# Performance work log

Measured on AMD Instinct MI355X. Metric: run time of the kernel, lower is better.

The kernel has to match this reference:

```python
import jax, jax.numpy as jnp
import numpy as np

N_HEADS = 16
ROPE_BASE = 10000.0


def _rotate_half(x):
    x1, x2 = jnp.split(x, 2, axis=-1)
    return jnp.concatenate([-x2, x1], axis=-1)


def _rope_cos_sin(positions, d_k, dtype):
    # standard YaRN-style rotary tables (attention scale mscale = 1.0)
    inv_freq = 1.0 / (ROPE_BASE ** (jnp.arange(0, d_k, 2, dtype=jnp.float32) / d_k))
    freqs = positions.astype(jnp.float32)[:, None] * inv_freq[None, :]  # [T, d_k/2]
    emb = jnp.concatenate([freqs, freqs], axis=-1)                      # [T, d_k]
    return jnp.cos(emb).astype(dtype), jnp.sin(emb).astype(dtype)


def setup_inputs() -> dict:
    key = jax.random.key(0)
    ks = jax.random.split(key, 8)
    B, T, D = 1, 2048, 1024
    s = 0.02
    return {
        "query": jax.random.normal(ks[0], (B, T, D), jnp.float32),
        "key": jax.random.normal(ks[1], (B, T, D), jnp.float32),
        "value": jax.random.normal(ks[2], (B, T, D), jnp.float32),
        "yarn_positions": jnp.arange(T, dtype=jnp.int32),
        "wq": jax.random.normal(ks[3], (D, D), jnp.float32) * s,
        "wk": jax.random.normal(ks[4], (D, D), jnp.float32) * s,
        "wv": jax.random.normal(ks[5], (D, D), jnp.float32) * s,
        "wo_w": jax.random.normal(ks[6], (D, D), jnp.float32) * s,
        "wo_b": jnp.zeros((D,), jnp.float32),
    }


def reference(query, key, value, yarn_positions, wq, wk, wv, wo_w, wo_b):
    B, Tq, D = query.shape
    Tk = key.shape[1]
    H = N_HEADS
    dk = D // H

    # nn.Linear(bias=False): y = x @ W.T
    Q = (query @ wq.T).reshape(B, Tq, H, dk).transpose(0, 2, 1, 3)  # [B,H,Tq,dk]
    K = (key @ wk.T).reshape(B, Tk, H, dk).transpose(0, 2, 1, 3)
    V = (value @ wv.T).reshape(B, Tk, H, dk).transpose(0, 2, 1, 3)

    # YaRN rotary position embedding on Q and K (same positions for q and k)
    cos, sin = _rope_cos_sin(yarn_positions, dk, Q.dtype)  # [T, dk]
    cos = cos[None, None, :, :]
    sin = sin[None, None, :, :]
    Q = Q * cos + _rotate_half(Q) * sin
    K = K * cos + _rotate_half(K) * sin

    scale = 1.0 / jnp.sqrt(jnp.asarray(dk, Q.dtype))
    scores = jnp.einsum('bhqd,bhkd->bhqk', Q, K) * scale  # [B,H,Tq,Tk]

    # causal mask (is_causal=True)
    causal = jnp.triu(jnp.ones((Tq, Tk), dtype=bool), 1)
    scores = jnp.where(causal[None, None], -jnp.inf, scores)

    attn = jax.nn.softmax(scores, axis=-1)
    out = jnp.einsum('bhqk,bhkd->bhqd', attn, V)
    out = out.transpose(0, 2, 1, 3).reshape(B, Tq, D)
    return out @ wo_w.T + wo_b
```

## Files before the change

kernel.cpp:

```cpp
#include <hip/hip_runtime.h>
#include <hip/hip_bf16.h>
#include <stdint.h>

#define TT 2048
#define DD 1024
#define NH 16
#define DK 64

typedef __attribute__((ext_vector_type(8))) short bf16x8;
typedef __attribute__((ext_vector_type(4))) float f32x4;
typedef __attribute__((ext_vector_type(8))) unsigned short u16x8;
typedef __attribute__((ext_vector_type(4))) unsigned short u16x4;

__device__ __forceinline__ unsigned short f2bf(float f) {
  union { float f; unsigned u; } x; x.f = f;
  unsigned r = (x.u + 0x7FFFu + ((x.u >> 16) & 1u)) >> 16;
  return (unsigned short)r;
}

__device__ __forceinline__ void gload16(const void* g, void* l) {
  __builtin_amdgcn_global_load_lds(
      (const __attribute__((address_space(1))) unsigned int*)g,
      (__attribute__((address_space(3))) unsigned int*)l, 16, 0, 0);
}

__global__ __launch_bounds__(256) void cvt_all(
    const float* __restrict__ q, const float* __restrict__ k, const float* __restrict__ v,
    const float* __restrict__ wq, const float* __restrict__ wk, const float* __restrict__ wv,
    const float* __restrict__ wo,
    unsigned short* __restrict__ oq, unsigned short* __restrict__ ok, unsigned short* __restrict__ ov,
    unsigned short* __restrict__ owq, unsigned short* __restrict__ owk, unsigned short* __restrict__ owv,
    unsigned short* __restrict__ owo) {
  int b = blockIdx.x;
  const float* src; unsigned short* dst; int sb;
  if (b < 1024)      { src = q;  dst = oq;  sb = b; }
  else if (b < 2048) { src = k;  dst = ok;  sb = b - 1024; }
  else if (b < 3072) { src = v;  dst = ov;  sb = b - 2048; }
  else if (b < 3584) { src = wq; dst = owq; sb = b - 3072; }
  else if (b < 4096) { src = wk; dst = owk; sb = b - 3584; }
  else if (b < 4608) { src = wv; dst = owv; sb = b - 4096; }
  else               { src = wo; dst = owo; sb = b - 4608; }
  size_t i0 = (size_t)sb * 2048 + (size_t)threadIdx.x * 8;
  f32x4 a = *(const f32x4*)(src + i0);
  f32x4 c = *(const f32x4*)(src + i0 + 4);
  u16x8 r;
#pragma unroll
  for (int j = 0; j < 4; ++j) { r[j] = f2bf(a[j]); r[j + 4] = f2bf(c[j]); }
  *(u16x8*)(dst + i0) = r;
}

__global__ __launch_bounds__(256) void rope_tab(const int* __restrict__ pos,
                                                float* __restrict__ cosT,
                                                float* __restrict__ sinT) {
  int idx = blockIdx.x * 256 + threadIdx.x;
  int t = idx >> 5, i = idx & 31;
  float inv = exp2f((float)i * -0.41524101186092028f);
  float ang = (float)pos[t] * inv;
  cosT[idx] = cosf(ang);
  sinT[idx] = sinf(ang);
}

__global__ __launch_bounds__(256) void gemm_qkv(
    const unsigned short* __restrict__ xq, const unsigned short* __restrict__ xk,
    const unsigned short* __restrict__ xv,
    const unsigned short* __restrict__ wqb, const unsigned short* __restrict__ wkb,
    const unsigned short* __restrict__ wvb,
    unsigned short* __restrict__ QF, unsigned short* __restrict__ KF,
    unsigned short* __restrict__ VF,
    const float* __restrict__ cosT, const float* __restrict__ sinT) {
  __shared__ unsigned short Ash[128 * 64];
  __shared__ unsigned short Bsh[128 * 64];
  const int z = blockIdx.z;
  const unsigned short* A = (z == 0) ? xq : (z == 1) ? xk : xv;
  const unsigned short* W = (z == 0) ? wqb : (z == 1) ? wkb : wvb;
  const int brow = blockIdx.x * 128;
  const int bcol = blockIdx.y * 128;
  const int tid = threadIdx.x;
  const int lane = tid & 63;
  const int w = tid >> 6;
  const int wr = w >> 1, wc = w & 1;
  const char* Ab = (const char*)A + (size_t)brow * (DD * 2);
  const char* Wb = (const char*)W + (size_t)bcol * (DD * 2);
  char* AshB = (char*)Ash;
  char* BshB = (char*)Bsh;
  f32x4 acc[4][4];
#pragma unroll
  for (int mi = 0; mi < 4; ++mi)
#pragma unroll
    for (int ni = 0; ni < 4; ++ni)
#pragma unroll
      for (int r = 0; r < 4; ++r) acc[mi][ni][r] = 0.0f;

  for (int k0 = 0; k0 < DD; k0 += 64) {
    __syncthreads();
#pragma unroll
    for (int it = 0; it < 4; ++it) {
      int c = it * 256 + tid;
      int row = c >> 3;
      int xb = (c & 7) << 4;
      int sxb = xb ^ ((row & 7) << 4);
      int ldso = (it * 256 + (tid & 192)) << 4;
      gload16(Ab + (size_t)row * (DD * 2) + k0 * 2 + sxb, AshB + ldso);
      gload16(Wb + (size_t)row * (DD * 2) + k0 * 2 + sxb, BshB + ldso);
    }
    __syncthreads();
#pragma unroll
    for (int ks = 0; ks < 2; ++ks) {
      bf16x8 af[4], bfr[4];
      int colb = ks * 64 + ((lane >> 4) << 4);
#pragma unroll
      for (int mi = 0; mi < 4; ++mi) {
        int row = wr * 64 + mi * 16 + (lane & 15);
        af[mi] = *(const bf16x8*)(AshB + row * 128 + (colb ^ ((row & 7) << 4)));
      }
#pragma unroll
      for (int ni = 0; ni < 4; ++ni) {
        int row = wc * 64 + ni * 16 + (lane & 15);
        bfr[ni] = *(const bf16x8*)(BshB + row * 128 + (colb ^ ((row & 7) << 4)));
      }
#pragma unroll
      for (int mi = 0; mi < 4; ++mi)
#pragma unroll
        for (int ni = 0; ni < 4; ++ni)
          acc[mi][ni] = __builtin_amdgcn_mfma_f32_16x16x32_bf16(af[mi], bfr[ni], acc[mi][ni], 0, 0, 0);
    }
  }

  const int hcol = bcol + wc * 64;
  const int h = hcol >> 6;
  if (z == 0) {
    const float sc = 0.18033688011112042f;
#pragma unroll
    for (int mi = 0; mi < 4; ++mi) {
#pragma unroll
      for (int r = 0; r < 4; ++r) {
        int t = brow + wr * 64 + mi * 16 + ((lane >> 4) << 2) + r;
        int qw_ = t >> 5, mif = (t >> 4) & 1, r16 = t & 15;
        size_t fb = (((size_t)(h * 64 + qw_) * 2 + mif) * 2) * 1024;
#pragma unroll
        for (int ni = 0; ni < 2; ++ni) {
          int dl = ni * 16 + (lane & 15);
          float cv = cosT[t * 32 + dl];
          float sv = sinT[t * 32 + dl];
          float x1 = acc[mi][ni][r];
          float x2 = acc[mi][ni + 2][r];
          size_t off = fb + (size_t)(r16 + 16 * (dl >> 3)) * 16 + (dl & 7) * 2;
          *(unsigned short*)((char*)QF + off) = f2bf((x1 * cv - x2 * sv) * sc);
          *(unsigned short*)((char*)QF + off + 1024) = f2bf((x2 * cv + x1 * sv) * sc);
        }
      }
    }
  } else if (z == 1) {
#pragma unroll
    for (int mi = 0; mi < 4; ++mi) {
#pragma unroll
      for (int r = 0; r < 4; ++r) {
        int t = brow + wr * 64 + mi * 16 + ((lane >> 4) << 2) + r;
        int kt = t >> 6, nif = (t >> 4) & 3, r16 = t & 15;
        size_t fb = (((size_t)(h * 32 + kt) * 2) * 4 + nif) * 1024;
#pragma unroll
        for (int ni = 0; ni < 2; ++ni) {
          int dl = ni * 16 + (lane & 15);
          float cv = cosT[t * 32 + dl];
          float sv = sinT[t * 32 + dl];
          float x1 = acc[mi][ni][r];
          float x2 = acc[mi][ni + 2][r];
          size_t off = fb + (size_t)(r16 + 16 * (dl >> 3)) * 16 + (dl & 7) * 2;
          *(unsigned short*)((char*)KF + off) = f2bf(x1 * cv - x2 * sv);
          *(unsigned short*)((char*)KF + off + 4096) = f2bf(x2 * cv + x1 * sv);
        }
      }
    }
  } else {
#pragma unroll
    for (int mi = 0; mi < 4; ++mi) {
      int t0 = brow + wr * 64 + mi * 16 + ((lane >> 4) << 2);
      int kt = t0 >> 6, ksf = (t0 & 63) >> 5, slot = (t0 & 31) >> 3, j0 = t0 & 7;
#pragma unroll
      for (int ni = 0; ni < 4; ++ni) {
        int dh = ni * 16 + (lane & 15);
        int lanef = (dh & 15) + 16 * slot;
        int nif = dh >> 4;
        size_t off = ((((size_t)(h * 32 + kt) * 2 + ksf) * 4 + nif) * 64 + lanef) * 16 + j0 * 2;
        u16x4 pk;
#pragma unroll
        for (int r = 0; r < 4; ++r) pk[r] = f2bf(acc[mi][ni][r]);
        *(u16x4*)((char*)VF + off) = pk;
      }
    }
  }
}

__global__ __launch_bounds__(256, 2) void attn_fa(
    const unsigned short* __restrict__ QF, const unsigned short* __restrict__ KF,
    const unsigned short* __restrict__ VF, unsigned short* __restrict__ AO) {
  __shared__ char LB[26624];
  __shared__ float MR[4][32];
  const int tid = threadIdx.x;
  const int lane = tid & 63;
  const int w = tid >> 6;
  const int bid = blockIdx.x;
  const int xcd = bid & 7;
  const int idx = bid >> 3;
  const int h = xcd * 2 + (idx & 1);
  const int qw = 63 - (idx >> 1);
  const int q0w = qw * 32;
  const int NT = (qw >> 1) + 1;
  char* PshB = LB + w * 4096;
  const char* Kb = (const char*)KF + (size_t)h * 32 * 8192;
  const char* Vb = (const char*)VF + (size_t)h * 32 * 8192;

  bf16x8 qf[2][2];
  {
    const char* Qb = (const char*)QF + (size_t)(h * 64 + qw) * 4096;
#pragma unroll
    for (int mi = 0; mi < 2; ++mi)
#pragma unroll
      for (int ks = 0; ks < 2; ++ks)
        qf[mi][ks] = *(const bf16x8*)(Qb + (mi * 2 + ks) * 1024 + lane * 16);
  }

  bf16x8 vone;
#pragma unroll
  for (int j = 0; j < 8; ++j) vone[j] = (short)0x3F80;

  f32x4 accO[2][5];
  float mrow[2];
#pragma unroll
  for (int mi = 0; mi < 2; ++mi) {
    mrow[mi] = -1e30f;
#pragma unroll
    for (int ni = 0; ni < 5; ++ni)
#pragma unroll
      for (int r = 0; r < 4; ++r) accO[mi][ni][r] = 0.0f;
  }

  bf16x8 kfA[2][4], kfB[2][4], vf[2][4];
  {
    int kt0 = (w < NT) ? w : 0;
    const char* p = Kb + (size_t)kt0 * 8192 + lane * 16;
#pragma unroll
    for (int ks = 0; ks < 2; ++ks)
#pragma unroll
      for (int ni = 0; ni < 4; ++ni)
        kfA[ks][ni] = *(const bf16x8*)(p + (ks * 4 + ni) * 1024);
  }

  for (int kt = w; kt < NT; kt += 4) {
    {
      const char* p = Vb + (size_t)kt * 8192 + lane * 16;
#pragma unroll
      for (int ks = 0; ks < 2; ++ks)
#pragma unroll
        for (int ni = 0; ni < 4; ++ni)
          vf[ks][ni] = *(const bf16x8*)(p + (ks * 4 + ni) * 1024);
    }
    f32x4 s[2][4];
#pragma unroll
    for (int mi = 0; mi < 2; ++mi)
#pragma unroll
      for (int ni = 0; ni < 4; ++ni)
#pragma unroll
        for (int r = 0; r < 4; ++r) s[mi][ni][r] = 0.0f;
    __builtin_amdgcn_s_setprio(1);
#pragma unroll
    for (int ks = 0; ks < 2; ++ks)
#pragma unroll
      for (int mi = 0; mi < 2; ++mi)
#pragma unroll
        for (int ni = 0; ni < 4; ++ni)
          s[mi][ni] = __builtin_amdgcn_mfma_f32_16x16x32_bf16(kfA[ks][ni], qf[mi][ks], s[mi][ni], 0, 0, 0);
    __builtin_amdgcn_s_setprio(0);
    if (kt + 4 < NT) {
      const char* p = Kb + (size_t)(kt + 4) * 8192 + lane * 16;
#pragma unroll
      for (int ks = 0; ks < 2; ++ks)
#pragma unroll
        for (int ni = 0; ni < 4; ++ni)
          kfB[ks][ni] = *(const bf16x8*)(p + (ks * 4 + ni) * 1024);
    }

    if (kt == NT - 1) {
#pragma unroll
      for (int mi = 0; mi < 2; ++mi) {
        int qq = q0w + mi * 16 + (lane & 15);
#pragma unroll
        for (int ni = 0; ni < 4; ++ni) {
          int kb = kt * 64 + ni * 16 + ((lane >> 4) << 2);
#pragma unroll
          for (int r = 0; r < 4; ++r)
            if (kb + r > qq) s[mi][ni][r] = -1e30f;
        }
      }
    }
    float rmx[2];
#pragma unroll
    for (int mi = 0; mi < 2; ++mi) {
      f32x4 t;
#pragma unroll
      for (int r = 0; r < 4; ++r)
        t[r] = fmaxf(fmaxf(s[mi][0][r], s[mi][1][r]), fmaxf(s[mi][2][r], s[mi][3][r]));
      float mx = fmaxf(fmaxf(t[0], t[1]), fmaxf(t[2], t[3]));
      mx = fmaxf(mx, __shfl_xor(mx, 16, 64));
      mx = fmaxf(mx, __shfl_xor(mx, 32, 64));
      rmx[mi] = mx;
    }
    bool need = (rmx[0] > mrow[0] + 8.0f) || (rmx[1] > mrow[1] + 8.0f);
    if (__any(need)) {
#pragma unroll
      for (int mi = 0; mi < 2; ++mi) {
        float mn = fmaxf(mrow[mi], rmx[mi]);
        float al = exp2f(mrow[mi] - mn);
        mrow[mi] = mn;
        float ar[4];
#pragma unroll
        for (int r = 0; r < 4; ++r) ar[r] = __shfl(al, ((lane >> 4) << 2) + r, 64);
#pragma unroll
        for (int ni = 0; ni < 5; ++ni)
#pragma unroll
          for (int r = 0; r < 4; ++r) accO[mi][ni][r] *= ar[r];
      }
    }
#pragma unroll
    for (int mi = 0; mi < 2; ++mi) {
      int row = mi * 16 + (lane & 15);
      int rbase = row * 128;
      int sw = (row & 7) << 4;
#pragma unroll
      for (int ni = 0; ni < 4; ++ni) {
        unsigned u0 = __float_as_uint(exp2f(s[mi][ni][0] - mrow[mi]));
        unsigned u1 = __float_as_uint(exp2f(s[mi][ni][1] - mrow[mi]));
        unsigned u2 = __float_as_uint(exp2f(s[mi][ni][2] - mrow[mi]));
        unsigned u3 = __float_as_uint(exp2f(s[mi][ni][3] - mrow[mi]));
        uint2 pk;
        pk.x = (u0 >> 16) | (u1 & 0xFFFF0000u);
        pk.y = (u2 >> 16) | (u3 & 0xFFFF0000u);
        int cb = ni * 32 + ((lane >> 4) << 3);
        *(uint2*)(PshB + rbase + (cb ^ sw)) = pk;
      }
    }
    asm volatile("" ::: "memory");
    __builtin_amdgcn_s_setprio(1);
#pragma unroll
    for (int ks = 0; ks < 2; ++ks) {
      bf16x8 pf[2];
#pragma unroll
      for (int mi = 0; mi < 2; ++mi) {
        int row = mi * 16 + (lane & 15);
        int cb = ks * 64 + ((lane >> 4) << 4);
        pf[mi] = *(const bf16x8*)(PshB + row * 128 + (cb ^ ((row & 7) << 4)));
      }
#pragma unroll
      for (int mi = 0; mi < 2; ++mi) {
#pragma unroll
        for (int ni = 0; ni < 4; ++ni)
          accO[mi][ni] = __builtin_amdgcn_mfma_f32_16x16x32_bf16(pf[mi], vf[ks][ni], accO[mi][ni], 0, 0, 0);
        accO[mi][4] = __builtin_amdgcn_mfma_f32_16x16x32_bf16(pf[mi], vone, accO[mi][4], 0, 0, 0);
      }
    }
    __builtin_amdgcn_s_setprio(0);
#pragma unroll
    for (int ks = 0; ks < 2; ++ks)
#pragma unroll
      for (int ni = 0; ni < 4; ++ni) kfA[ks][ni] = kfB[ks][ni];
  }

  __syncthreads();
  if ((lane >> 4) == 0) {
    MR[w][lane] = mrow[0];
    MR[w][16 + lane] = mrow[1];
  }
  if (w > 0) {
    float* MOw = (float*)LB + (size_t)(w - 1) * 32 * 68;
#pragma unroll
    for (int mi = 0; mi < 2; ++mi) {
#pragma unroll
      for (int r = 0; r < 4; ++r) {
        int rq = mi * 16 + ((lane >> 4) << 2) + r;
#pragma unroll
        for (int ni = 0; ni < 4; ++ni)
          MOw[rq * 68 + ni * 16 + (lane & 15)] = accO[mi][ni][r];
        if ((lane & 15) == 0) MOw[rq * 68 + 64] = accO[mi][4][r];
      }
    }
  }
  __syncthreads();
  if (w == 0) {
    const float* MOp = (const float*)LB;
#pragma unroll
    for (int mi = 0; mi < 2; ++mi) {
#pragma unroll
      for (int r = 0; r < 4; ++r) {
        int rq = mi * 16 + ((lane >> 4) << 2) + r;
        float m0 = MR[0][rq], m1 = MR[1][rq], m2 = MR[2][rq], m3 = MR[3][rq];
        float M = fmaxf(fmaxf(m0, m1), fmaxf(m2, m3));
        float a0 = exp2f(m0 - M), a1 = exp2f(m1 - M);
        float a2 = exp2f(m2 - M), a3 = exp2f(m3 - M);
        float denom = a0 * accO[mi][4][r] + a1 * MOp[(0 * 32 + rq) * 68 + 64] +
                      a2 * MOp[(1 * 32 + rq) * 68 + 64] + a3 * MOp[(2 * 32 + rq) * 68 + 64];
        float inv = 1.0f / denom;
        int t = q0w + rq;
#pragma unroll
        for (int ni = 0; ni < 4; ++ni) {
          int dh = ni * 16 + (lane & 15);
          float o = a0 * accO[mi][ni][r] + a1 * MOp[(0 * 32 + rq) * 68 + dh] +
                    a2 * MOp[(1 * 32 + rq) * 68 + dh] + a3 * MOp[(2 * 32 + rq) * 68 + dh];
          AO[(size_t)t * DD + h * DK + dh] = f2bf(o * inv);
        }
      }
    }
  }
}

__global__ __launch_bounds__(256) void gemm_o(
    const unsigned short* __restrict__ A, const unsigned short* __restrict__ W,
    const float* __restrict__ bias, float* __restrict__ out) {
  __shared__ unsigned short Ash[128 * 64];
  __shared__ unsigned short Bsh[128 * 64];
  const int brow = blockIdx.x * 128;
  const int bcol = blockIdx.y * 128;
  const int tid = threadIdx.x;
  const int lane = tid & 63;
  const int w = tid >> 6;
  const int wr = w >> 1, wc = w & 1;
  const char* Ab = (const char*)A + (size_t)brow * (DD * 2);
  const char* Wb = (const char*)W + (size_t)bcol * (DD * 2);
  char* AshB = (char*)Ash;
  char* BshB = (char*)Bsh;
  f32x4 acc[4][4];
#pragma unroll
  for (int mi = 0; mi < 4; ++mi)
#pragma unroll
    for (int ni = 0; ni < 4; ++ni)
#pragma unroll
      for (int r = 0; r < 4; ++r) acc[mi][ni][r] = 0.0f;

  for (int k0 = 0; k0 < DD; k0 += 64) {
    __syncthreads();
#pragma unroll
    for (int it = 0; it < 4; ++it) {
      int c = it * 256 + tid;
      int row = c >> 3;
      int xb = (c & 7) << 4;
      int sxb = xb ^ ((row & 7) << 4);
      int ldso = (it * 256 + (tid & 192)) << 4;
      gload16(Ab + (size_t)row * (DD * 2) + k0 * 2 + sxb, AshB + ldso);
      gload16(Wb + (size_t)row * (DD * 2) + k0 * 2 + sxb, BshB + ldso);
    }
    __syncthreads();
#pragma unroll
    for (int ks = 0; ks < 2; ++ks) {
      bf16x8 af[4], bfr[4];
      int colb = ks * 64 + ((lane >> 4) << 4);
#pragma unroll
      for (int mi = 0; mi < 4; ++mi) {
        int row = wr * 64 + mi * 16 + (lane & 15);
        af[mi] = *(const bf16x8*)(AshB + row * 128 + (colb ^ ((row & 7) << 4)));
      }
#pragma unroll
      for (int ni = 0; ni < 4; ++ni) {
        int row = wc * 64 + ni * 16 + (lane & 15);
        bfr[ni] = *(const bf16x8*)(BshB + row * 128 + (colb ^ ((row & 7) << 4)));
      }
#pragma unroll
      for (int mi = 0; mi < 4; ++mi)
#pragma unroll
        for (int ni = 0; ni < 4; ++ni)
          acc[mi][ni] = __builtin_amdgcn_mfma_f32_16x16x32_bf16(af[mi], bfr[ni], acc[mi][ni], 0, 0, 0);
    }
  }
#pragma unroll
  for (int mi = 0; mi < 4; ++mi)
#pragma unroll
    for (int r = 0; r < 4; ++r) {
      int t = brow + wr * 64 + mi * 16 + ((lane >> 4) << 2) + r;
#pragma unroll
      for (int ni = 0; ni < 4; ++ni) {
        int o = bcol + wc * 64 + ni * 16 + (lane & 15);
        out[(size_t)t * DD + o] = acc[mi][ni][r] + bias[o];
      }
    }
}

extern "C" void kernel_launch(void* const* d_in, const int* in_sizes, int n_in,
                              void* d_out, int out_size, void* d_ws, size_t ws_size,
                              hipStream_t stream) {
  const float* q  = (const float*)d_in[0];
  const float* k  = (const float*)d_in[1];
  const float* v  = (const float*)d_in[2];
  const int* pos  = (const int*)d_in[3];
  const float* wq = (const float*)d_in[4];
  const float* wk = (const float*)d_in[5];
  const float* wv = (const float*)d_in[6];
  const float* wo = (const float*)d_in[7];
  const float* wob = (const float*)d_in[8];
  float* out = (float*)d_out;
  char* ws = (char*)d_ws;

  const size_t MB = 1u << 20;
  unsigned short* XQ = (unsigned short*)(ws + 0 * MB);
  unsigned short* XK = (unsigned short*)(ws + 4 * MB);
  unsigned short* XV = (unsigned short*)(ws + 8 * MB);
  unsigned short* WQ = (unsigned short*)(ws + 12 * MB);
  unsigned short* WK = (unsigned short*)(ws + 14 * MB);
  unsigned short* WV = (unsigned short*)(ws + 16 * MB);
  unsigned short* WO = (unsigned short*)(ws + 18 * MB);
  unsigned short* QF = (unsigned short*)(ws + 20 * MB);
  unsigned short* KF = (unsigned short*)(ws + 24 * MB);
  unsigned short* VF = (unsigned short*)(ws + 28 * MB);
  unsigned short* AOb = (unsigned short*)(ws + 32 * MB);
  float* COS = (float*)(ws + 36 * MB);
  float* SIN = (float*)(ws + 36 * MB + 262144);

  hipLaunchKernelGGL(cvt_all, dim3(5120), dim3(256), 0, stream,
                     q, k, v, wq, wk, wv, wo, XQ, XK, XV, WQ, WK, WV, WO);
  hipLaunchKernelGGL(rope_tab, dim3(256), dim3(256), 0, stream, pos, COS, SIN);
  hipLaunchKernelGGL(gemm_qkv, dim3(16, 8, 3), dim3(256), 0, stream,
                     XQ, XK, XV, WQ, WK, WV, QF, KF, VF, COS, SIN);
  hipLaunchKernelGGL(attn_fa, dim3(1024), dim3(256), 0, stream, QF, KF, VF, AOb);
  hipLaunchKernelGGL(gemm_o, dim3(16, 8), dim3(256), 0, stream, AOb, WO, wob, out);
}
```

Measured before the change: 84.65 us.

## Fuse fp32-to-bf16 conversion into GEMM staging and shrink GEMM tiles

New measurement: 95.06 us. 1.12x slower.

```diff
diff --git a/kernel.cpp b/kernel.cpp
--- a/kernel.cpp
+++ b/kernel.cpp
@@ -9,6 +9,7 @@
 
 typedef __attribute__((ext_vector_type(8))) short bf16x8;
 typedef __attribute__((ext_vector_type(4))) float f32x4;
+typedef __attribute__((ext_vector_type(4))) unsigned uint4v;
 typedef __attribute__((ext_vector_type(8))) unsigned short u16x8;
 typedef __attribute__((ext_vector_type(4))) unsigned short u16x4;
 
@@ -18,35 +19,16 @@
   return (unsigned short)r;
 }
 
+__device__ __forceinline__ unsigned cvt2(float lo, float hi) {
+  unsigned r;
+  asm("v_cvt_pk_bf16_f32 %0, %1, %2" : "=v"(r) : "v"(lo), "v"(hi));
+  return r;
+}
+
 __device__ __forceinline__ void gload16(const void* g, void* l) {
   __builtin_amdgcn_global_load_lds(
       (const __attribute__((address_space(1))) unsigned int*)g,
       (__attribute__((address_space(3))) unsigned int*)l, 16, 0, 0);
-}
-
-__global__ __launch_bounds__(256) void cvt_all(
-    const float* __restrict__ q, const float* __restrict__ k, const float* __restrict__ v,
-    const float* __restrict__ wq, const float* __restrict__ wk, const float* __restrict__ wv,
-    const float* __restrict__ wo,
-    unsigned short* __restrict__ oq, unsigned short* __restrict__ ok, unsigned short* __restrict__ ov,
-    unsigned short* __restrict__ owq, unsigned short* __restrict__ owk, unsigned short* __restrict__ owv,
-    unsigned short* __restrict__ owo) {
-  int b = blockIdx.x;
-  const float* src; unsigned short* dst; int sb;
-  if (b < 1024)      { src = q;  dst = oq;  sb = b; }
-  else if (b < 2048) { src = k;  dst = ok;  sb = b - 1024; }
-  else if (b < 3072) { src = v;  dst = ov;  sb = b - 2048; }
-  else if (b < 3584) { src = wq; dst = owq; sb = b - 3072; }
-  else if (b < 4096) { src = wk; dst = owk; sb = b - 3584; }
-  else if (b < 4608) { src = wv; dst = owv; sb = b - 4096; }
-  else               { src = wo; dst = owo; sb = b - 4608; }
-  size_t i0 = (size_t)sb * 2048 + (size_t)threadIdx.x * 8;
-  f32x4 a = *(const f32x4*)(src + i0);
-  f32x4 c = *(const f32x4*)(src + i0 + 4);
-  u16x8 r;
-#pragma unroll
-  for (int j = 0; j < 4; ++j) { r[j] = f2bf(a[j]); r[j + 4] = f2bf(c[j]); }
-  *(u16x8*)(dst + i0) = r;
 }
 
 __global__ __launch_bounds__(256) void rope_tab(const int* __restrict__ pos,
@@ -60,32 +42,49 @@
   sinT[idx] = sinf(ang);
 }
 
+template <int ITERS>
+__device__ __forceinline__ void stage_f32(const float* __restrict__ src0,
+                                          char* lds, int tid) {
+#pragma unroll
+  for (int it = 0; it < ITERS; ++it) {
+    int c = it * 256 + tid;
+    int row = c >> 3;
+    int col8 = (c & 7) * 8;
+    const float* s = src0 + (size_t)row * DD + col8;
+    f32x4 a = *(const f32x4*)s;
+    f32x4 b = *(const f32x4*)(s + 4);
+    uint4v pk;
+    pk[0] = cvt2(a[0], a[1]);
+    pk[1] = cvt2(a[2], a[3]);
+    pk[2] = cvt2(b[0], b[1]);
+    pk[3] = cvt2(b[2], b[3]);
+    *(uint4v*)(lds + row * 128 + ((col8 * 2) ^ ((row & 7) << 4))) = pk;
+  }
+}
+
 __global__ __launch_bounds__(256) void gemm_qkv(
-    const unsigned short* __restrict__ xq, const unsigned short* __restrict__ xk,
-    const unsigned short* __restrict__ xv,
-    const unsigned short* __restrict__ wqb, const unsigned short* __restrict__ wkb,
-    const unsigned short* __restrict__ wvb,
+    const float* __restrict__ xq, const float* __restrict__ xk,
+    const float* __restrict__ xv,
+    const float* __restrict__ wqf, const float* __restrict__ wkf,
+    const float* __restrict__ wvf,
     unsigned short* __restrict__ QF, unsigned short* __restrict__ KF,
     unsigned short* __restrict__ VF,
     const float* __restrict__ cosT, const float* __restrict__ sinT) {
   __shared__ unsigned short Ash[128 * 64];
-  __shared__ unsigned short Bsh[128 * 64];
+  __shared__ unsigned short Bsh[64 * 64];
   const int z = blockIdx.z;
-  const unsigned short* A = (z == 0) ? xq : (z == 1) ? xk : xv;
-  const unsigned short* W = (z == 0) ? wqb : (z == 1) ? wkb : wvb;
+  const float* A = (z == 0) ? xq : (z == 1) ? xk : xv;
+  const float* W = (z == 0) ? wqf : (z == 1) ? wkf : wvf;
   const int brow = blockIdx.x * 128;
-  const int bcol = blockIdx.y * 128;
+  const int h = blockIdx.y;
   const int tid = threadIdx.x;
   const int lane = tid & 63;
   const int w = tid >> 6;
-  const int wr = w >> 1, wc = w & 1;
-  const char* Ab = (const char*)A + (size_t)brow * (DD * 2);
-  const char* Wb = (const char*)W + (size_t)bcol * (DD * 2);
   char* AshB = (char*)Ash;
   char* BshB = (char*)Bsh;
-  f32x4 acc[4][4];
-#pragma unroll
-  for (int mi = 0; mi < 4; ++mi)
+  f32x4 acc[2][4];
+#pragma unroll
+  for (int mi = 0; mi < 2; ++mi)
 #pragma unroll
     for (int ni = 0; ni < 4; ++ni)
 #pragma unroll
@@ -93,48 +92,38 @@
 
   for (int k0 = 0; k0 < DD; k0 += 64) {
     __syncthreads();
-#pragma unroll
-    for (int it = 0; it < 4; ++it) {
-      int c = it * 256 + tid;
-      int row = c >> 3;
-      int xb = (c & 7) << 4;
-      int sxb = xb ^ ((row & 7) << 4);
-      int ldso = (it * 256 + (tid & 192)) << 4;
-      gload16(Ab + (size_t)row * (DD * 2) + k0 * 2 + sxb, AshB + ldso);
-      gload16(Wb + (size_t)row * (DD * 2) + k0 * 2 + sxb, BshB + ldso);
-    }
+    stage_f32<4>(A + (size_t)brow * DD + k0, AshB, tid);
+    stage_f32<2>(W + (size_t)h * 64 * DD + k0, BshB, tid);
     __syncthreads();
 #pragma unroll
     for (int ks = 0; ks < 2; ++ks) {
-      bf16x8 af[4], bfr[4];
+      bf16x8 af[2], bfr[4];
       int colb = ks * 64 + ((lane >> 4) << 4);
 #pragma unroll
-      for (int mi = 0; mi < 4; ++mi) {
-        int row = wr * 64 + mi * 16 + (lane & 15);
+      for (int mi = 0; mi < 2; ++mi) {
+        int row = w * 32 + mi * 16 + (lane & 15);
         af[mi] = *(const bf16x8*)(AshB + row * 128 + (colb ^ ((row & 7) << 4)));
       }
 #pragma unroll
       for (int ni = 0; ni < 4; ++ni) {
-        int row = wc * 64 + ni * 16 + (lane & 15);
+        int row = ni * 16 + (lane & 15);
         bfr[ni] = *(const bf16x8*)(BshB + row * 128 + (colb ^ ((row & 7) << 4)));
       }
 #pragma unroll
-      for (int mi = 0; mi < 4; ++mi)
+      for (int mi = 0; mi < 2; ++mi)
 #pragma unroll
         for (int ni = 0; ni < 4; ++ni)
           acc[mi][ni] = __builtin_amdgcn_mfma_f32_16x16x32_bf16(af[mi], bfr[ni], acc[mi][ni], 0, 0, 0);
     }
   }
 
-  const int hcol = bcol + wc * 64;
-  const int h = hcol >> 6;
   if (z == 0) {
     const float sc = 0.18033688011112042f;
 #pragma unroll
-    for (int mi = 0; mi < 4; ++mi) {
+    for (int mi = 0; mi < 2; ++mi) {
 #pragma unroll
       for (int r = 0; r < 4; ++r) {
-        int t = brow + wr * 64 + mi * 16 + ((lane >> 4) << 2) + r;
+        int t = brow + w * 32 + mi * 16 + ((lane >> 4) << 2) + r;
         int qw_ = t >> 5, mif = (t >> 4) & 1, r16 = t & 15;
         size_t fb = (((size_t)(h * 64 + qw_) * 2 + mif) * 2) * 1024;
 #pragma unroll
@@ -152,10 +141,10 @@
     }
   } else if (z == 1) {
 #pragma unroll
-    for (int mi = 0; mi < 4; ++mi) {
+    for (int mi = 0; mi < 2; ++mi) {
 #pragma unroll
       for (int r = 0; r < 4; ++r) {
-        int t = brow + wr * 64 + mi * 16 + ((lane >> 4) << 2) + r;
+        int t = brow + w * 32 + mi * 16 + ((lane >> 4) << 2) + r;
         int kt = t >> 6, nif = (t >> 4) & 3, r16 = t & 15;
         size_t fb = (((size_t)(h * 32 + kt) * 2) * 4 + nif) * 1024;
 #pragma unroll
@@ -173,15 +162,14 @@
     }
   } else {
 #pragma unroll
-    for (int mi = 0; mi < 4; ++mi) {
-      int t0 = brow + wr * 64 + mi * 16 + ((lane >> 4) << 2);
+    for (int mi = 0; mi < 2; ++mi) {
+      int t0 = brow + w * 32 + mi * 16 + ((lane >> 4) << 2);
       int kt = t0 >> 6, ksf = (t0 & 63) >> 5, slot = (t0 & 31) >> 3, j0 = t0 & 7;
 #pragma unroll
       for (int ni = 0; ni < 4; ++ni) {
         int dh = ni * 16 + (lane & 15);
         int lanef = (dh & 15) + 16 * slot;
-        int nif = dh >> 4;
-        size_t off = ((((size_t)(h * 32 + kt) * 2 + ksf) * 4 + nif) * 64 + lanef) * 16 + j0 * 2;
+        size_t off = ((((size_t)(h * 32 + kt) * 2 + ksf) * 4 + ni) * 64 + lanef) * 16 + j0 * 2;
         u16x4 pk;
 #pragma unroll
         for (int r = 0; r < 4; ++r) pk[r] = f2bf(acc[mi][ni][r]);
@@ -413,23 +401,21 @@
 }
 
 __global__ __launch_bounds__(256) void gemm_o(
-    const unsigned short* __restrict__ A, const unsigned short* __restrict__ W,
+    const unsigned short* __restrict__ A, const float* __restrict__ Wf,
     const float* __restrict__ bias, float* __restrict__ out) {
   __shared__ unsigned short Ash[128 * 64];
-  __shared__ unsigned short Bsh[128 * 64];
+  __shared__ unsigned short Bsh[64 * 64];
   const int brow = blockIdx.x * 128;
-  const int bcol = blockIdx.y * 128;
+  const int bcol = blockIdx.y * 64;
   const int tid = threadIdx.x;
   const int lane = tid & 63;
   const int w = tid >> 6;
-  const int wr = w >> 1, wc = w & 1;
   const char* Ab = (const char*)A + (size_t)brow * (DD * 2);
-  const char* Wb = (const char*)W + (size_t)bcol * (DD * 2);
   char* AshB = (char*)Ash;
   char* BshB = (char*)Bsh;
-  f32x4 acc[4][4];
-#pragma unroll
-  for (int mi = 0; mi < 4; ++mi)
+  f32x4 acc[2][4];
+#pragma unroll
+  for (int mi = 0; mi < 2; ++mi)
 #pragma unroll
     for (int ni = 0; ni < 4; ++ni)
 #pragma unroll
@@ -445,38 +431,38 @@
       int sxb = xb ^ ((row & 7) << 4);
       int ldso = (it * 256 + (tid & 192)) << 4;
       gload16(Ab + (size_t)row * (DD * 2) + k0 * 2 + sxb, AshB + ldso);
-      gload16(Wb + (size_t)row * (DD * 2) + k0 * 2 + sxb, BshB + ldso);
-    }
+    }
+    stage_f32<2>(Wf + (size_t)bcol * DD + k0, BshB, tid);
     __syncthreads();
 #pragma unroll
     for (int ks = 0; ks < 2; ++ks) {
-      bf16x8 af[4], bfr[4];
+      bf16x8 af[2], bfr[4];
       int colb = ks * 64 + ((lane >> 4) << 4);
 #pragma unroll
-      for (int mi = 0; mi < 4; ++mi) {
-        int row = wr * 64 + mi * 16 + (lane & 15);
+      for (int mi = 0; mi < 2; ++mi) {
+        int row = w * 32 + mi * 16 + (lane & 15);
         af[mi] = *(const bf16x8*)(AshB + row * 128 + (colb ^ ((row & 7) << 4)));
       }
 #pragma unroll
       for (int ni = 0; ni < 4; ++ni) {
-        int row = wc * 64 + ni * 16 + (lane & 15);
+        int row = ni * 16 + (lane & 15);
         bfr[ni] = *(const bf16x8*)(BshB + row * 128 + (colb ^ ((row & 7) << 4)));
       }
 #pragma unroll
-      for (int mi = 0; mi < 4; ++mi)
+      for (int mi = 0; mi < 2; ++mi)
 #pragma unroll
         for (int ni = 0; ni < 4; ++ni)
           acc[mi][ni] = __builtin_amdgcn_mfma_f32_16x16x32_bf16(af[mi], bfr[ni], acc[mi][ni], 0, 0, 0);
     }
   }
 #pragma unroll
-  for (int mi = 0; mi < 4; ++mi)
+  for (int mi = 0; mi < 2; ++mi)
 #pragma unroll
     for (int r = 0; r < 4; ++r) {
-      int t = brow + wr * 64 + mi * 16 + ((lane >> 4) << 2) + r;
+      int t = brow + w * 32 + mi * 16 + ((lane >> 4) << 2) + r;
 #pragma unroll
       for (int ni = 0; ni < 4; ++ni) {
-        int o = bcol + wc * 64 + ni * 16 + (lane & 15);
+        int o = bcol + ni * 16 + (lane & 15);
         out[(size_t)t * DD + o] = acc[mi][ni][r] + bias[o];
       }
     }
@@ -498,25 +484,16 @@
   char* ws = (char*)d_ws;
 
   const size_t MB = 1u << 20;
-  unsigned short* XQ = (unsigned short*)(ws + 0 * MB);
-  unsigned short* XK = (unsigned short*)(ws + 4 * MB);
-  unsigned short* XV = (unsigned short*)(ws + 8 * MB);
-  unsigned short* WQ = (unsigned short*)(ws + 12 * MB);
-  unsigned short* WK = (unsigned short*)(ws + 14 * MB);
-  unsigned short* WV = (unsigned short*)(ws + 16 * MB);
-  unsigned short* WO = (unsigned short*)(ws + 18 * MB);
-  unsigned short* QF = (unsigned short*)(ws + 20 * MB);
-  unsigned short* KF = (unsigned short*)(ws + 24 * MB);
-  unsigned short* VF = (unsigned short*)(ws + 28 * MB);
-  unsigned short* AOb = (unsigned short*)(ws + 32 * MB);
-  float* COS = (float*)(ws + 36 * MB);
-  float* SIN = (float*)(ws + 36 * MB + 262144);
-
-  hipLaunchKernelGGL(cvt_all, dim3(5120), dim3(256), 0, stream,
-                     q, k, v, wq, wk, wv, wo, XQ, XK, XV, WQ, WK, WV, WO);
+  unsigned short* QF = (unsigned short*)(ws + 0 * MB);
+  unsigned short* KF = (unsigned short*)(ws + 4 * MB);
+  unsigned short* VF = (unsigned short*)(ws + 8 * MB);
+  unsigned short* AOb = (unsigned short*)(ws + 12 * MB);
+  float* COS = (float*)(ws + 16 * MB);
+  float* SIN = (float*)(ws + 16 * MB + 262144);
+
   hipLaunchKernelGGL(rope_tab, dim3(256), dim3(256), 0, stream, pos, COS, SIN);
-  hipLaunchKernelGGL(gemm_qkv, dim3(16, 8, 3), dim3(256), 0, stream,
-                     XQ, XK, XV, WQ, WK, WV, QF, KF, VF, COS, SIN);
+  hipLaunchKernelGGL(gemm_qkv, dim3(16, 16, 3), dim3(256), 0, stream,
+                     q, k, v, wq, wk, wv, QF, KF, VF, COS, SIN);
   hipLaunchKernelGGL(attn_fa, dim3(1024), dim3(256), 0, stream, QF, KF, VF, AOb);
-  hipLaunchKernelGGL(gemm_o, dim3(16, 8), dim3(256), 0, stream, AOb, WO, wob, out);
-}
+  hipLaunchKernelGGL(gemm_o, dim3(16, 16), dim3(256), 0, stream, AOb, wo, wob, out);
+}
```
